# Kernel optimization log

Hardware: AMD Instinct MI355X
Metric: run time of the kernel (lower is better)

## Reference

```python
import jax, jax.numpy as jnp
import numpy as np

N = 50000      # total packed nodes
E = 1600000    # edges (no self loops; layers add them)
G = 64         # graphs in the batch
F_IN = 24      # raw node feature dim
D = 64         # hidden dim
H = 4          # attention heads
C = D // H     # 16 channels per head
L = 3          # GAT layers
NEG = 0.2      # LeakyReLU negative slope (GATv2 default)
EPS = 1e-5     # LayerNorm eps


def setup_inputs() -> dict:
    key = jax.random.key(0)
    ks = jax.random.split(key, 16)
    x = jax.random.normal(ks[0], (N, F_IN), jnp.float32)
    src = jax.random.randint(ks[1], (E,), 0, N)
    dst = jax.random.randint(ks[2], (E,), 0, N)
    dst = jnp.where(dst == src, (dst + 1) % N, dst)  # keep edge list self-loop free
    edge_index = jnp.stack([src, dst]).astype(jnp.int32)
    batch = jnp.sort(jax.random.randint(ks[3], (N,), 0, G)).astype(jnp.int32)
    s = 0.1
    return dict(
        x=x, edge_index=edge_index, batch=batch,
        w_in=jax.random.normal(ks[4], (F_IN, D), jnp.float32) * s,
        b_in=jnp.zeros((D,), jnp.float32),
        w_l=jax.random.normal(ks[5], (L, D, D), jnp.float32) * s,
        b_l=jnp.zeros((L, D), jnp.float32),
        w_r=jax.random.normal(ks[6], (L, D, D), jnp.float32) * s,
        b_r=jnp.zeros((L, D), jnp.float32),
        att=jax.random.normal(ks[7], (L, H, C), jnp.float32) * s,
        b_gat=jnp.zeros((L, D), jnp.float32),
        ln_g=jnp.ones((L, D), jnp.float32),
        ln_b=jnp.zeros((L, D), jnp.float32),
        w_g1=jax.random.normal(ks[8], (D, D // 2), jnp.float32) * s,
        b_g1=jnp.zeros((D // 2,), jnp.float32),
        w_g2=jax.random.normal(ks[9], (D // 2, 1), jnp.float32) * s,
        b_g2=jnp.zeros((1,), jnp.float32),
        w_out=jax.random.normal(ks[10], (D, D), jnp.float32) * s,
        b_out=jnp.zeros((D,), jnp.float32),
    )


def _layernorm(h, g, b):
    m = h.mean(-1, keepdims=True)
    v = ((h - m) ** 2).mean(-1, keepdims=True)
    return (h - m) * jax.lax.rsqrt(v + EPS) * g + b


def _gatv2(h, src, dst, wl, bl, wr, br, att, bg):
    n = h.shape[0]
    xl = (h @ wl + bl).reshape(n, H, C)   # source transform
    xr = (h @ wr + br).reshape(n, H, C)   # target transform
    # edge scores: att . leaky_relu(xl[j] + xr[i])  -> [E', H]
    e = jnp.sum(jax.nn.leaky_relu(xl[src] + xr[dst], NEG) * att, axis=-1)
    emax = jax.ops.segment_max(e, dst, num_segments=n)
    ex = jnp.exp(e - emax[dst])
    denom = jax.ops.segment_sum(ex, dst, num_segments=n)
    alpha = ex / denom[dst]               # segment softmax over incoming edges
    out = jax.ops.segment_sum(alpha[:, :, None] * xl[src], dst, num_segments=n)
    return out.reshape(n, D) + bg


def reference(x, edge_index, batch, w_in, b_in, w_l, b_l, w_r, b_r, att, b_gat,
              ln_g, ln_b, w_g1, b_g1, w_g2, b_g2, w_out, b_out):
    n = x.shape[0]
    loops = jnp.arange(n, dtype=edge_index.dtype)
    src = jnp.concatenate([edge_index[0], loops])  # add self loops once
    dst = jnp.concatenate([edge_index[1], loops])
    h = jax.nn.relu(x @ w_in + b_in)
    for i in range(L):
        res = h
        h = _gatv2(h, src, dst, w_l[i], b_l[i], w_r[i], b_r[i], att[i], b_gat[i])
        h = _layernorm(h + res, ln_g[i], ln_b[i])
        if i < L - 1:
            h = jax.nn.relu(h)
    # GlobalAttention pooling: gate MLP -> per-graph softmax -> weighted sum
    gate = jax.nn.relu(h @ w_g1 + b_g1) @ w_g2 + b_g2  # [N, 1]
    gmax = jax.ops.segment_max(gate, batch, num_segments=G)
    ge = jnp.exp(gate - gmax[batch])
    gs = jax.ops.segment_sum(ge, batch, num_segments=G)
    a = ge / jnp.where(gs > 0, gs, 1.0)[batch]
    emb = jax.ops.segment_sum(a * h, batch, num_segments=G)  # [G, D]
    return jax.nn.relu(emb @ w_out + b_out)
```

## Files before the change

kernel.cpp:

```cpp
#include <hip/hip_runtime.h>

#define NEGS   0.2f
#define LN_EPS 1e-5f
#define BSH    7
#define BN     128
#define TILE   4096
#define LOG2E  1.44269504f

typedef const float* __restrict__ fp;
typedef _Float16 v2h __attribute__((ext_vector_type(2)));
typedef _Float16 v8h __attribute__((ext_vector_type(8)));
typedef float    v4f __attribute__((ext_vector_type(4)));

__device__ __forceinline__ v2h u2h(unsigned u){ union{unsigned u; v2h h;} c; c.u = u; return c.h; }
__device__ __forceinline__ unsigned h2u(v2h h){ union{v2h h; unsigned u;} c; c.h = h; return c.u; }

template<int CTRL>
__device__ __forceinline__ float dppadd(float x){
  int y = __builtin_amdgcn_update_dpp(0, __float_as_int(x), CTRL, 0xF, 0xF, true);
  return x + __int_as_float(y);
}

__device__ __forceinline__ float dot8(v8h a, v8h b, float init){
  union U { v8h v; v2h h[4]; };
  U ua; ua.v = a;
  U ub; ub.v = b;
  float s = init;
  #pragma unroll
  for (int i = 0; i < 4; ++i) s = __builtin_amdgcn_fdot2(ua.h[i], ub.h[i], s, false);
  return s;
}

__device__ __forceinline__ v8h leaky8(v8h t){
  return __builtin_elementwise_max(t, t * (_Float16)NEGS);
}

__device__ __forceinline__ float edge_w8(v8h v, v8h xr8, v8h att8, float negm2){
  v8h t = leaky8(v + xr8);
  float s = dppadd<0xB1>(dot8(t, att8, negm2));
  return __builtin_amdgcn_exp2f(s);
}

__global__ __launch_bounds__(256) void k_in(fp x, fp w, fp b, float* __restrict__ h,
                                            unsigned* __restrict__ h16, int N){
  __shared__ float ws[24*64];
  __shared__ float bs[64];
  __shared__ float xs[4][24];
  int tid = threadIdx.x;
  for (int i = tid; i < 24*64; i += 256) ws[i] = w[i];
  if (tid < 64) bs[tid] = b[tid];
  int r = tid >> 6, c = tid & 63;
  int row = blockIdx.x*4 + r;
  if (c < 24 && row < N) xs[r][c] = x[row*24 + c];
  __syncthreads();
  float acc = bs[c];
  #pragma unroll
  for (int k = 0; k < 24; ++k) acc = fmaf(xs[r][k], ws[k*64 + c], acc);
  float y = fmaxf(acc, 0.f);
  float y1 = __shfl_down(y, 1);
  if (row < N){
    h[(size_t)row*64 + c] = y;
    if (!(c & 1)){
      v2h p; p.x = (_Float16)y; p.y = (_Float16)y1;
      h16[(size_t)row*32 + (c >> 1)] = h2u(p);
    }
  }
}

__global__ __launch_bounds__(256) void k_wprep(fp w_l, fp w_r, fp att, _Float16* __restrict__ wf,
                                               _Float16* __restrict__ att16){
  int lm = blockIdx.x;
  if (lm < 3){
    for (int d = threadIdx.x; d < 64; d += 256)
      att16[lm*64 + d] = (_Float16)(att[lm*64 + d] * LOG2E);
  }
  const float* src = ((lm & 1) ? w_r : w_l) + (lm >> 1)*4096;
  _Float16* dst = wf + lm*4096;
  for (int d = threadIdx.x; d < 4096; d += 256){
    int j = d & 7, l = (d >> 3) & 63, kc = (d >> 9) & 1, nt = d >> 10;
    int k = kc*32 + (l >> 4)*8 + j;
    int n = nt*16 + (l & 15);
    dst[d] = (_Float16)src[k*64 + n];
  }
}

__global__ __launch_bounds__(256) void t_hist(const int* __restrict__ dstA, int* __restrict__ counts,
                                              int E, int K, int ntiles){
  __shared__ int hist[512];
  int t = blockIdx.x, tid = threadIdx.x;
  for (int i = tid; i < K; i += 256) hist[i] = 0;
  __syncthreads();
  int e0 = t*TILE, e1 = min(e0 + TILE, E);
  for (int e = e0 + tid; e < e1; e += 256)
    atomicAdd(&hist[dstA[e] >> BSH], 1);
  __syncthreads();
  for (int i = tid; i < K; i += 256) counts[i*ntiles + t] = hist[i];
}

__global__ __launch_bounds__(512) void s_scan_tiles(int* __restrict__ counts, int* __restrict__ btotal,
                                                    int ntiles){
  __shared__ int s[512];
  int b = blockIdx.x, tid = threadIdx.x;
  int v = (tid < ntiles) ? counts[b*ntiles + tid] : 0;
  s[tid] = v;
  __syncthreads();
  for (int off = 1; off < 512; off <<= 1){
    int t = (tid >= off) ? s[tid - off] : 0;
    __syncthreads();
    s[tid] += t;
    __syncthreads();
  }
  if (tid < ntiles) counts[b*ntiles + tid] = s[tid] - v;
  if (tid == 511) btotal[b] = s[511];
}

__global__ __launch_bounds__(512) void s_scan_buckets(const int* __restrict__ btotal,
                                                      int* __restrict__ bbase, int K, int E){
  __shared__ int s[512];
  int tid = threadIdx.x;
  int v = (tid < K) ? btotal[tid] : 0;
  s[tid] = v;
  __syncthreads();
  for (int off = 1; off < 512; off <<= 1){
    int t = (tid >= off) ? s[tid - off] : 0;
    __syncthreads();
    s[tid] += t;
    __syncthreads();
  }
  if (tid < K) bbase[tid] = s[tid] - v;
  if (tid == 0) bbase[K] = E;
}

__global__ __launch_bounds__(256) void t_scatter(const int* __restrict__ srcA, const int* __restrict__ dstA,
                                                 const int* __restrict__ counts, const int* __restrict__ bbase,
                                                 unsigned* __restrict__ packed, int E, int K, int ntiles){
  __shared__ int gb[512];
  __shared__ int cur[512];
  int t = blockIdx.x, tid = threadIdx.x;
  for (int i = tid; i < K; i += 256){
    gb[i] = bbase[i] + counts[i*ntiles + t];
    cur[i] = 0;
  }
  __syncthreads();
  int e0 = t*TILE, e1 = min(e0 + TILE, E);
  for (int e = e0 + tid; e < e1; e += 256){
    int d = dstA[e], sv = srcA[e];
    int b = d >> BSH;
    int p = atomicAdd(&cur[b], 1);
    packed[gb[b] + p] = ((unsigned)(d & (BN-1)) << 25) | (unsigned)sv;
  }
}

__global__ __launch_bounds__(256) void k_fine(const unsigned* __restrict__ packed, const int* __restrict__ bbase,
                                              int* __restrict__ row_ptr, int* __restrict__ col, int N, int K){
  __shared__ int hist[BN];
  __shared__ int excl[BN];
  int b = blockIdx.x, tid = threadIdx.x;
  int node0 = b << BSH;
  int e_base = bbase[b], e_end = bbase[b+1];
  if (tid < BN) hist[tid] = 0;
  __syncthreads();
  for (int e = e_base + tid; e < e_end; e += 256)
    atomicAdd(&hist[packed[e] >> 25], 1);
  __syncthreads();
  int v = (tid < BN) ? hist[tid] : 0;
  if (tid < BN) excl[tid] = v;
  __syncthreads();
  for (int off = 1; off < BN; off <<= 1){
    int t2 = 0;
    if (tid < BN && tid >= off) t2 = excl[tid - off];
    __syncthreads();
    if (tid < BN) excl[tid] += t2;
    __syncthreads();
  }
  int nn = min(BN, N - node0);
  if (tid < nn) row_ptr[node0 + tid] = e_base + excl[tid] - v;
  if (b == K-1 && tid == 0) row_ptr[N] = e_end;
  if (tid < BN) hist[tid] = excl[tid] - v;
  __syncthreads();
  for (int e = e_base + tid; e < e_end; e += 256){
    unsigned u = packed[e];
    int dl = u >> 25;
    int p = atomicAdd(&hist[dl], 1);
    col[e_base + p] = (int)(u & 0x1FFFFFFu);
  }
}

__global__ __launch_bounds__(256) void k_xfm(const unsigned* __restrict__ h16,
                                             const _Float16* __restrict__ wf,
                                             fp blg, fp brg,
                                             unsigned* __restrict__ xl16, unsigned* __restrict__ xr16, int N){
  int tid = threadIdx.x, wave = tid >> 6, lane = tid & 63;
  int quad = lane >> 4, ln = lane & 15;
  int m0 = blockIdx.x*64 + wave*16;
  if (m0 >= N) return;
  int m = m0 + ln;
  bool mv = m < N;
  v8h a0 = {}, a1 = {};
  if (mv){
    a0 = *(const v8h*)&h16[(size_t)m*32 + quad*4];
    a1 = *(const v8h*)&h16[(size_t)m*32 + 16 + quad*4];
  }
  #pragma unroll
  for (int mat = 0; mat < 2; ++mat){
    const _Float16* wb = wf + mat*4096;
    fp bias = mat ? brg : blg;
    unsigned* dst = mat ? xr16 : xl16;
    #pragma unroll
    for (int nt = 0; nt < 4; ++nt){
      v8h b0 = *(const v8h*)&wb[nt*1024 + lane*8];
      v8h b1 = *(const v8h*)&wb[nt*1024 + 512 + lane*8];
      float bv = bias[nt*16 + ln];
      v4f acc = {bv, bv, bv, bv};
      acc = __builtin_amdgcn_mfma_f32_16x16x32_f16(a0, b0, acc, 0, 0, 0);
      acc = __builtin_amdgcn_mfma_f32_16x16x32_f16(a1, b1, acc, 0, 0, 0);
      #pragma unroll
      for (int r = 0; r < 4; ++r){
        float partner = __shfl_xor(acc[r], 1);
        int node = m0 + quad*4 + r;
        if (!(lane & 1) && node < N){
          v2h p; p.x = (_Float16)acc[r]; p.y = (_Float16)partner;
          dst[(size_t)node*32 + nt*8 + (ln >> 1)] = h2u(p);
        }
      }
    }
  }
}

__global__ __launch_bounds__(256) void k_gat(const unsigned* __restrict__ xl16, const unsigned* __restrict__ xr16,
                                             float* __restrict__ h, unsigned* __restrict__ h16,
                                             const int* __restrict__ row_ptr, const int* __restrict__ col,
                                             const _Float16* __restrict__ att16, fp bg, fp lng, fp lnb,
                                             int N, int do_relu){
  int lane = threadIdx.x & 63;
  int node = blockIdx.x*4 + (threadIdx.x >> 6);
  if (node >= N) return;
  int g = lane >> 3;
  int s = lane & 7;

  v8h att8 = *(const v8h*)&att16[s*8];
  v8h xr8  = *(const v8h*)&xr16[(size_t)node*32 + s*4];
  v8h xl8  = *(const v8h*)&xl16[(size_t)node*32 + s*4];

  float m = dppadd<0xB1>(dot8(leaky8(xl8 + xr8), att8, 0.f));
  float negm2 = m * -0.5f;

  float den = (g == 0) ? 1.f : 0.f;
  float acc[8];
  #pragma unroll
  for (int i = 0; i < 8; ++i) acc[i] = (g == 0) ? (float)xl8[i] : 0.f;

  int e = row_ptr[node], e1 = row_ptr[node+1];
  for (; e + 16 <= e1; e += 16){
    int j0 = col[e + g];
    int j1 = col[e + 8 + g];
    v8h v0 = *(const v8h*)&xl16[(size_t)j0*32 + s*4];
    v8h v1 = *(const v8h*)&xl16[(size_t)j1*32 + s*4];
    float w0 = edge_w8(v0, xr8, att8, negm2);
    float w1 = edge_w8(v1, xr8, att8, negm2);
    den += w0; den += w1;
    #pragma unroll
    for (int i = 0; i < 8; ++i){
      acc[i] = fmaf(w0, (float)v0[i], acc[i]);
      acc[i] = fmaf(w1, (float)v1[i], acc[i]);
    }
  }
  for (; e < e1; e += 8){
    int idx = e + g;
    bool valid = idx < e1;
    int j0 = col[valid ? idx : e];
    v8h v0 = *(const v8h*)&xl16[(size_t)j0*32 + s*4];
    float w0 = edge_w8(v0, xr8, att8, negm2);
    w0 = valid ? w0 : 0.f;
    den += w0;
    #pragma unroll
    for (int i = 0; i < 8; ++i) acc[i] = fmaf(w0, (float)v0[i], acc[i]);
  }

  #pragma unroll
  for (int o = 8; o < 64; o <<= 1){
    den += __shfl_xor(den, o);
    #pragma unroll
    for (int i = 0; i < 8; ++i) acc[i] += __shfl_xor(acc[i], o);
  }
  float inv = 1.f / den;

  float4 bgA = *(const float4*)&bg[s*8];
  float4 bgB = *(const float4*)&bg[s*8 + 4];
  float4 hA  = *(const float4*)&h[(size_t)node*64 + s*8];
  float4 hB  = *(const float4*)&h[(size_t)node*64 + s*8 + 4];
  float res8[8] = {hA.x + bgA.x, hA.y + bgA.y, hA.z + bgA.z, hA.w + bgA.w,
                   hB.x + bgB.x, hB.y + bgB.y, hB.z + bgB.z, hB.w + bgB.w};
  float o8[8];
  float sl = 0.f;
  #pragma unroll
  for (int i = 0; i < 8; ++i){ o8[i] = fmaf(acc[i], inv, res8[i]); sl += o8[i]; }
  #pragma unroll
  for (int o = 1; o < 8; o <<= 1) sl += __shfl_xor(sl, o);
  float mean = sl * (1.f/64.f);
  float vsl = 0.f;
  #pragma unroll
  for (int i = 0; i < 8; ++i){ o8[i] -= mean; vsl = fmaf(o8[i], o8[i], vsl); }
  #pragma unroll
  for (int o = 1; o < 8; o <<= 1) vsl += __shfl_xor(vsl, o);
  float rs = rsqrtf(vsl * (1.f/64.f) + LN_EPS);

  if (g == 0){
    float4 lgA = *(const float4*)&lng[s*8], lgB = *(const float4*)&lng[s*8 + 4];
    float4 lbA = *(const float4*)&lnb[s*8], lbB = *(const float4*)&lnb[s*8 + 4];
    float lg8[8] = {lgA.x, lgA.y, lgA.z, lgA.w, lgB.x, lgB.y, lgB.z, lgB.w};
    float lb8[8] = {lbA.x, lbA.y, lbA.z, lbA.w, lbB.x, lbB.y, lbB.z, lbB.w};
    float y[8];
    #pragma unroll
    for (int i = 0; i < 8; ++i){
      y[i] = fmaf(o8[i]*rs, lg8[i], lb8[i]);
      if (do_relu) y[i] = fmaxf(y[i], 0.f);
    }
    float4 yA = {y[0], y[1], y[2], y[3]};
    float4 yB = {y[4], y[5], y[6], y[7]};
    *(float4*)&h[(size_t)node*64 + s*8]     = yA;
    *(float4*)&h[(size_t)node*64 + s*8 + 4] = yB;
    v8h p;
    #pragma unroll
    for (int i = 0; i < 8; ++i) p[i] = (_Float16)y[i];
    *(v8h*)&h16[(size_t)node*32 + s*4] = p;
  }
}

__global__ __launch_bounds__(256) void k_gate(const float* __restrict__ h, fp w1, fp b1, fp w2, fp b2,
                                              float* __restrict__ gate, int N){
  __shared__ float w1s[2048];
  __shared__ float hrow[16][64];
  int tid = threadIdx.x;
  for (int i = tid*4; i < 2048; i += 1024) *(float4*)&w1s[i] = *(const float4*)&w1[i];
  int base = blockIdx.x*16;
  int nrows = min(16, N - base);
  int lim = nrows*64;
  for (int i = tid*4; i < lim; i += 1024)
    *(float4*)&hrow[0][i] = *(const float4*)&h[(size_t)base*64 + i];
  __syncthreads();
  int wave = tid >> 6, lane = tid & 63;
  int j = lane & 31, half = lane >> 5;
  float b1v = b1[j], w2v = w2[j], b2v = b2[0];
  int k0 = half*32;
  #pragma unroll
  for (int it = 0; it < 4; ++it){
    int r = wave*4 + it;
    int node = base + r;
    if (node >= N) break;
    float s = 0.f;
    #pragma unroll 8
    for (int k = k0; k < k0 + 32; ++k) s = fmaf(hrow[r][k], w1s[k*32 + j], s);
    s += __shfl_xor(s, 32);
    float hid = fmaxf(s + b1v, 0.f);
    float contrib = (half == 0) ? hid * w2v : 0.f;
    #pragma unroll
    for (int o = 1; o < 64; o <<= 1) contrib += __shfl_xor(contrib, o);
    if (lane == 0) gate[node] = contrib + b2v;
  }
}

__global__ __launch_bounds__(256) void k_gmax(const float* __restrict__ gate, const int* __restrict__ batch,
                                              float* __restrict__ gmax, float* __restrict__ gsum,
                                              float* __restrict__ embsum, int N){
  int g = blockIdx.x, tid = threadIdx.x;
  if (tid < 64) embsum[g*64 + tid] = 0.f;
  if (tid == 64) gsum[g] = 0.f;
  int lo = 0, hi = N;
  while (lo < hi){ int mid = (lo + hi) >> 1; if (batch[mid] < g) lo = mid + 1; else hi = mid; }
  int start = lo;
  hi = N;
  while (lo < hi){ int mid = (lo + hi) >> 1; if (batch[mid] < g + 1) lo = mid + 1; else hi = mid; }
  int end = lo;
  float m = -3.4e38f;
  for (int i = start + tid; i < end; i += 256) m = fmaxf(m, gate[i]);
  #pragma unroll
  for (int o = 1; o < 64; o <<= 1) m = fmaxf(m, __shfl_xor(m, o));
  __shared__ float ws[4];
  if ((tid & 63) == 0) ws[tid >> 6] = m;
  __syncthreads();
  if (tid == 0) gmax[g] = fmaxf(fmaxf(ws[0], ws[1]), fmaxf(ws[2], ws[3]));
}

__global__ __launch_bounds__(256) void k_emb(const float* __restrict__ h, const float* __restrict__ gate,
                                             const int* __restrict__ batch, const float* __restrict__ gmax,
                                             float* __restrict__ gsum, float* __restrict__ embsum, int N){
  int lane = threadIdx.x & 63;
  int wv = blockIdx.x*4 + (threadIdx.x >> 6);
  int s = wv*64;
  if (s >= N) return;
  int e = min(s + 64, N);
  int cur = batch[s];
  float gm = gmax[cur];
  float acc = 0.f, asum = 0.f;
  for (int i = s; i < e; ++i){
    int g = batch[i];
    if (g != cur){
      atomicAdd(&embsum[cur*64 + lane], acc);
      if (lane == 0) atomicAdd(&gsum[cur], asum);
      acc = 0.f; asum = 0.f; cur = g; gm = gmax[g];
    }
    float a = __expf(gate[i] - gm);
    acc = fmaf(a, h[(size_t)i*64 + lane], acc);
    asum += a;
  }
  atomicAdd(&embsum[cur*64 + lane], acc);
  if (lane == 0) atomicAdd(&gsum[cur], asum);
}

__global__ __launch_bounds__(64) void k_out(const float* __restrict__ embsum, const float* __restrict__ gsum,
                                            fp w_out, fp b_out, float* __restrict__ out, int G){
  int g = blockIdx.x, lane = threadIdx.x;
  __shared__ float emb[64];
  float gs = gsum[g];
  float inv = (gs > 0.f) ? 1.f/gs : 1.f;
  emb[lane] = embsum[g*64 + lane] * inv;
  __syncthreads();
  float o2 = b_out[lane];
  #pragma unroll 8
  for (int d = 0; d < 64; ++d) o2 = fmaf(emb[d], w_out[d*64 + lane], o2);
  out[g*64 + lane] = fmaxf(o2, 0.f);
}

extern "C" void kernel_launch(void* const* d_in, const int* in_sizes, int n_in,
                              void* d_out, int out_size, void* d_ws, size_t ws_size,
                              hipStream_t stream) {
  const int N = in_sizes[0] / 24;
  const int E = in_sizes[1] / 2;
  const int G = out_size / 64;
  const int K = (N + BN - 1) >> BSH;
  const int ntiles = (E + TILE - 1) / TILE;

  fp x      = (fp)d_in[0];
  const int* edge  = (const int*)d_in[1];
  const int* batch = (const int*)d_in[2];
  fp w_in   = (fp)d_in[3];
  fp b_in   = (fp)d_in[4];
  fp w_l    = (fp)d_in[5];
  fp b_l    = (fp)d_in[6];
  fp w_r    = (fp)d_in[7];
  fp b_r    = (fp)d_in[8];
  fp att    = (fp)d_in[9];
  fp b_gat  = (fp)d_in[10];
  fp ln_g   = (fp)d_in[11];
  fp ln_b   = (fp)d_in[12];
  fp w_g1   = (fp)d_in[13];
  fp b_g1   = (fp)d_in[14];
  fp w_g2   = (fp)d_in[15];
  fp b_g2   = (fp)d_in[16];
  fp w_out  = (fp)d_in[17];
  fp b_out  = (fp)d_in[18];
  float* out = (float*)d_out;

  char* wp = (char*)d_ws;
  auto alloc = [&](size_t bytes) -> char* {
    char* p = wp; wp += (bytes + 255) & ~(size_t)255; return p;
  };
  float*    h       = (float*)    alloc((size_t)N*64*sizeof(float));
  unsigned* h16     = (unsigned*) alloc((size_t)N*32*sizeof(unsigned));
  unsigned* xl16    = (unsigned*) alloc((size_t)N*32*sizeof(unsigned));
  unsigned* xr16    = (unsigned*) alloc((size_t)N*32*sizeof(unsigned));
  int*      col     = (int*)      alloc((size_t)E*sizeof(int));
  unsigned* packed  = (unsigned*) alloc((size_t)E*sizeof(unsigned));
  int*      counts  = (int*)      alloc((size_t)K*ntiles*sizeof(int));
  int*      btotal  = (int*)      alloc((size_t)K*sizeof(int));
  int*      bbase   = (int*)      alloc((size_t)(K+1)*sizeof(int));
  int*      row_ptr = (int*)      alloc((size_t)(N+1)*sizeof(int));
  float*    gate    = (float*)    alloc((size_t)N*sizeof(float));
  float*    gmax    = (float*)    alloc((size_t)G*sizeof(float));
  float*    gsum    = (float*)    alloc((size_t)(G + G*64)*sizeof(float));
  float*    embsum  = gsum + G;
  _Float16* wf      = (_Float16*) alloc((size_t)3*2*4096*sizeof(_Float16));
  _Float16* att16g  = (_Float16*) alloc((size_t)3*64*sizeof(_Float16));

  const int* srcA = edge;
  const int* dstA = edge + E;

  k_in<<<(N + 3)/4, 256, 0, stream>>>(x, w_in, b_in, h, h16, N);
  k_wprep<<<6, 256, 0, stream>>>(w_l, w_r, att, wf, att16g);

  t_hist<<<ntiles, 256, 0, stream>>>(dstA, counts, E, K, ntiles);
  s_scan_tiles<<<K, 512, 0, stream>>>(counts, btotal, ntiles);
  s_scan_buckets<<<1, 512, 0, stream>>>(btotal, bbase, K, E);
  t_scatter<<<ntiles, 256, 0, stream>>>(srcA, dstA, counts, bbase, packed, E, K, ntiles);
  k_fine<<<K, 256, 0, stream>>>(packed, bbase, row_ptr, col, N, K);

  for (int i = 0; i < 3; ++i){
    k_xfm<<<(N + 63)/64, 256, 0, stream>>>(h16, wf + i*8192, b_l + i*64, b_r + i*64,
                                           xl16, xr16, N);
    k_gat<<<(N + 3)/4, 256, 0, stream>>>(xl16, xr16, h, h16, row_ptr, col,
                                         att16g + i*64, b_gat + i*64, ln_g + i*64, ln_b + i*64,
                                         N, i < 2 ? 1 : 0);
  }
  k_gate<<<(N + 15)/16, 256, 0, stream>>>(h, w_g1, b_g1, w_g2, b_g2, gate, N);
  k_gmax<<<G, 256, 0, stream>>>(gate, batch, gmax, gsum, embsum, N);
  k_emb<<<(N + 255)/256, 256, 0, stream>>>(h, gate, batch, gmax, gsum, embsum, N);
  k_out<<<G, 64, 0, stream>>>(embsum, gsum, w_out, b_out, out, G);
}
```

Measured before the change: 360.8 us.

## Map eight nodes per wavefront in GAT aggregation and shrink pooling chunks

Result: faster. 344.9 us (-4.4%).

```diff
diff --git a/kernel.cpp b/kernel.cpp
--- a/kernel.cpp
+++ b/kernel.cpp
@@ -19,6 +19,12 @@
 __device__ __forceinline__ float dppadd(float x){
   int y = __builtin_amdgcn_update_dpp(0, __float_as_int(x), CTRL, 0xF, 0xF, true);
   return x + __int_as_float(y);
+}
+__device__ __forceinline__ float hsum8(float s){
+  s = dppadd<0xB1>(s);
+  s = dppadd<0x4E>(s);
+  s = dppadd<0x141>(s);
+  return s;
 }
 
 __device__ __forceinline__ float dot8(v8h a, v8h b, float init){
@@ -233,79 +239,70 @@
                                              const _Float16* __restrict__ att16, fp bg, fp lng, fp lnb,
                                              int N, int do_relu){
   int lane = threadIdx.x & 63;
-  int node = blockIdx.x*4 + (threadIdx.x >> 6);
-  if (node >= N) return;
   int g = lane >> 3;
   int s = lane & 7;
+  int node = (blockIdx.x*4 + (threadIdx.x >> 6))*8 + g;
+  bool valid = node < N;
+  int nodec = valid ? node : N - 1;
 
   v8h att8 = *(const v8h*)&att16[s*8];
-  v8h xr8  = *(const v8h*)&xr16[(size_t)node*32 + s*4];
-  v8h xl8  = *(const v8h*)&xl16[(size_t)node*32 + s*4];
+  v8h xr8  = *(const v8h*)&xr16[(size_t)nodec*32 + s*4];
+  v8h xl8  = *(const v8h*)&xl16[(size_t)nodec*32 + s*4];
 
   float m = dppadd<0xB1>(dot8(leaky8(xl8 + xr8), att8, 0.f));
   float negm2 = m * -0.5f;
 
-  float den = (g == 0) ? 1.f : 0.f;
+  float den = 1.f;
   float acc[8];
   #pragma unroll
-  for (int i = 0; i < 8; ++i) acc[i] = (g == 0) ? (float)xl8[i] : 0.f;
-
-  int e = row_ptr[node], e1 = row_ptr[node+1];
-  for (; e + 16 <= e1; e += 16){
-    int j0 = col[e + g];
-    int j1 = col[e + 8 + g];
+  for (int i = 0; i < 8; ++i) acc[i] = (float)xl8[i];
+
+  int e  = row_ptr[nodec];
+  int e1 = valid ? row_ptr[nodec + 1] : e;
+
+  for (; e + 2 <= e1; e += 2){
+    int j0 = col[e], j1 = col[e+1];
     v8h v0 = *(const v8h*)&xl16[(size_t)j0*32 + s*4];
     v8h v1 = *(const v8h*)&xl16[(size_t)j1*32 + s*4];
     float w0 = edge_w8(v0, xr8, att8, negm2);
     float w1 = edge_w8(v1, xr8, att8, negm2);
-    den += w0; den += w1;
+    den += w0 + w1;
     #pragma unroll
     for (int i = 0; i < 8; ++i){
       acc[i] = fmaf(w0, (float)v0[i], acc[i]);
       acc[i] = fmaf(w1, (float)v1[i], acc[i]);
     }
   }
-  for (; e < e1; e += 8){
-    int idx = e + g;
-    bool valid = idx < e1;
-    int j0 = col[valid ? idx : e];
+  if (e < e1){
+    int j0 = col[e];
     v8h v0 = *(const v8h*)&xl16[(size_t)j0*32 + s*4];
     float w0 = edge_w8(v0, xr8, att8, negm2);
-    w0 = valid ? w0 : 0.f;
     den += w0;
     #pragma unroll
     for (int i = 0; i < 8; ++i) acc[i] = fmaf(w0, (float)v0[i], acc[i]);
   }
 
-  #pragma unroll
-  for (int o = 8; o < 64; o <<= 1){
-    den += __shfl_xor(den, o);
-    #pragma unroll
-    for (int i = 0; i < 8; ++i) acc[i] += __shfl_xor(acc[i], o);
-  }
   float inv = 1.f / den;
 
   float4 bgA = *(const float4*)&bg[s*8];
   float4 bgB = *(const float4*)&bg[s*8 + 4];
-  float4 hA  = *(const float4*)&h[(size_t)node*64 + s*8];
-  float4 hB  = *(const float4*)&h[(size_t)node*64 + s*8 + 4];
+  float4 hA  = *(const float4*)&h[(size_t)nodec*64 + s*8];
+  float4 hB  = *(const float4*)&h[(size_t)nodec*64 + s*8 + 4];
   float res8[8] = {hA.x + bgA.x, hA.y + bgA.y, hA.z + bgA.z, hA.w + bgA.w,
                    hB.x + bgB.x, hB.y + bgB.y, hB.z + bgB.z, hB.w + bgB.w};
   float o8[8];
   float sl = 0.f;
   #pragma unroll
   for (int i = 0; i < 8; ++i){ o8[i] = fmaf(acc[i], inv, res8[i]); sl += o8[i]; }
-  #pragma unroll
-  for (int o = 1; o < 8; o <<= 1) sl += __shfl_xor(sl, o);
+  sl = hsum8(sl);
   float mean = sl * (1.f/64.f);
   float vsl = 0.f;
   #pragma unroll
   for (int i = 0; i < 8; ++i){ o8[i] -= mean; vsl = fmaf(o8[i], o8[i], vsl); }
-  #pragma unroll
-  for (int o = 1; o < 8; o <<= 1) vsl += __shfl_xor(vsl, o);
+  vsl = hsum8(vsl);
   float rs = rsqrtf(vsl * (1.f/64.f) + LN_EPS);
 
-  if (g == 0){
+  if (valid){
     float4 lgA = *(const float4*)&lng[s*8], lgB = *(const float4*)&lng[s*8 + 4];
     float4 lbA = *(const float4*)&lnb[s*8], lbB = *(const float4*)&lnb[s*8 + 4];
     float lg8[8] = {lgA.x, lgA.y, lgA.z, lgA.w, lgB.x, lgB.y, lgB.z, lgB.w};
@@ -387,9 +384,9 @@
                                              float* __restrict__ gsum, float* __restrict__ embsum, int N){
   int lane = threadIdx.x & 63;
   int wv = blockIdx.x*4 + (threadIdx.x >> 6);
-  int s = wv*64;
+  int s = wv*16;
   if (s >= N) return;
-  int e = min(s + 64, N);
+  int e = min(s + 16, N);
   int cur = batch[s];
   float gm = gmax[cur];
   float acc = 0.f, asum = 0.f;
@@ -488,12 +485,12 @@
   for (int i = 0; i < 3; ++i){
     k_xfm<<<(N + 63)/64, 256, 0, stream>>>(h16, wf + i*8192, b_l + i*64, b_r + i*64,
                                            xl16, xr16, N);
-    k_gat<<<(N + 3)/4, 256, 0, stream>>>(xl16, xr16, h, h16, row_ptr, col,
-                                         att16g + i*64, b_gat + i*64, ln_g + i*64, ln_b + i*64,
-                                         N, i < 2 ? 1 : 0);
+    k_gat<<<(N + 31)/32, 256, 0, stream>>>(xl16, xr16, h, h16, row_ptr, col,
+                                           att16g + i*64, b_gat + i*64, ln_g + i*64, ln_b + i*64,
+                                           N, i < 2 ? 1 : 0);
   }
   k_gate<<<(N + 15)/16, 256, 0, stream>>>(h, w_g1, b_g1, w_g2, b_g2, gate, N);
   k_gmax<<<G, 256, 0, stream>>>(gate, batch, gmax, gsum, embsum, N);
-  k_emb<<<(N + 255)/256, 256, 0, stream>>>(h, gate, batch, gmax, gsum, embsum, N);
+  k_emb<<<(N + 255)/64, 256, 0, stream>>>(h, gate, batch, gmax, gsum, embsum, N);
   k_out<<<G, 64, 0, stream>>>(embsum, gsum, w_out, b_out, out, G);
 }
```
